# Performance work log

Hardware: AMD Instinct MI355X
Metric: run time of the kernel (lower is better)

The kernel has to match this reference:

```python
import jax, jax.numpy as jnp
import numpy as np

HID = 10  # hidden_dim


def conv1x1(x, w, b=None):
    # x: [N,C,H,W], w: [O,C] -> [N,O,H,W]
    y = jnp.einsum('oc,nchw->nohw', w, x)
    if b is not None:
        y = y + b[None, :, None, None]
    return y


def gconv1x1(x, w, b=None):
    # grouped 1x1 conv. x: [N,G*ipg,H,W], w: [G,opg,ipg]
    N, C, H, W = x.shape
    G, opg, ipg = w.shape
    xg = x.reshape(N, G, ipg, H, W)
    y = jnp.einsum('goi,ngihw->ngohw', w, xg).reshape(N, G * opg, H, W)
    if b is not None:
        y = y + b[None, :, None, None]
    return y


def _decomp(h_fea, xf, xh, att_w, att_b, w):
    # Decomposition: spatial attention from (fea, xf, xh), gate xf, project.
    att = jax.nn.sigmoid(conv1x1(jnp.concatenate([h_fea, xf, xh], axis=1), att_w, att_b))
    xfh = jax.nn.relu(conv1x1(xf * att, w))
    return xfh, att


def _comp(parts, xh, att_w, att_b, w):
    # Composition: parts [P,N,HID,H,W]; grouped per-part attention then fuse with xh.
    ca = jax.nn.sigmoid(jnp.einsum('pc,pnchw->pnhw', att_w[:, 0], parts) + att_b[:, None, None, None])
    msg = (parts * ca[:, :, None]).sum(0)  # [N,HID,H,W]
    return jax.nn.relu(conv1x1(jnp.concatenate([xh, msg], axis=1), w))


def _update(xh, m0, m1, m2, gate_w, gate_b, cand_w):
    # conv_Update: gated residual update from summed messages.
    cat = jnp.concatenate([xh, m0 + m1 + m2], axis=1)
    g = jax.nn.sigmoid(conv1x1(cat, gate_w, gate_b))
    cand = jax.nn.relu(conv1x1(cat, cand_w))
    return xh * (1.0 - g) + cand * g


def half_graph(h_fea, xh_u, xh_l, xf, xp, pdp_w1, pdp_w2, att_w, att_b,
               compU_att_w, compU_att_b, compU_w,
               compL_att_w, compL_att_b, compL_w,
               decU_att_w, decU_att_b, decU_w,
               decL_att_w, decL_att_b, decL_w,
               updU_gate_w, updU_gate_b, updU_cand_w,
               updL_gate_w, updL_gate_b, updL_cand_w):
    # Part_Dependency: shared trunk then grouped conv -> (dp_u, dp_l)
    t = jax.nn.relu(conv1x1(jnp.concatenate([h_fea, xh_u, xh_l], axis=1), pdp_w1))
    dp = jax.nn.relu(gconv1x1(t, pdp_w2))
    dp_u, dp_l = dp[:, :HID], dp[:, HID:]
    # grouped sigmoid attention over the two half nodes
    a = jax.nn.sigmoid(gconv1x1(jnp.concatenate([xh_u, xh_l], axis=1), att_w, att_b))
    ag_u, ag_l = a[:, 0:1], a[:, 1:2]
    # upper half node
    xphu = _comp(xp[0:4], xh_u, compU_att_w, compU_att_b, compU_w)
    xlh = dp_l * ag_l + xh_u * ag_u  # Pair_Part_Dependency (lower -> upper)
    xfhu, att_u = _decomp(h_fea, xf, xh_u, decU_att_w, decU_att_b, decU_w)
    xh_u_new = _update(xh_u, xphu, xlh, xfhu, updU_gate_w, updU_gate_b, updU_cand_w)
    # lower half node
    xphl = _comp(xp[4:6], xh_l, compL_att_w, compL_att_b, compL_w)
    xuh = dp_u * ag_u + xh_l * ag_l  # Pair_Part_Dependency (upper -> lower)
    xfhl, att_l = _decomp(h_fea, xf, xh_l, decL_att_w, decL_att_b, decL_w)
    xh_l_new = _update(xh_l, xphl, xuh, xfhl, updL_gate_w, updL_gate_b, updL_cand_w)
    return xh_u_new, xh_l_new, att_u, att_l


def setup_inputs() -> dict:
    key = jax.random.key(0)
    N, C, H, W = 8, 256, 128, 128
    ks = jax.random.split(key, 32)
    s = 0.05
    inp = {
        'h_fea': jax.random.normal(ks[0], (N, C, H, W), jnp.float32),
        'xh_u': jax.random.normal(ks[1], (N, HID, H, W), jnp.float32),
        'xh_l': jax.random.normal(ks[2], (N, HID, H, W), jnp.float32),
        'xf': jax.random.normal(ks[3], (N, HID, H, W), jnp.float32),
        'xp': jax.random.normal(ks[4], (6, N, HID, H, W), jnp.float32),
        'pdp_w1': jax.random.normal(ks[5], (2 * HID, C + 2 * HID), jnp.float32) * s,
        'pdp_w2': jax.random.normal(ks[6], (2, HID, HID), jnp.float32) * s,
        'att_w': jax.random.normal(ks[7], (2, 1, HID), jnp.float32) * s,
        'att_b': jnp.zeros((2,), jnp.float32),
        'compU_att_w': jax.random.normal(ks[8], (4, 1, HID), jnp.float32) * s,
        'compU_att_b': jnp.zeros((4,), jnp.float32),
        'compU_w': jax.random.normal(ks[9], (HID, 2 * HID), jnp.float32) * s,
        'compL_att_w': jax.random.normal(ks[10], (2, 1, HID), jnp.float32) * s,
        'compL_att_b': jnp.zeros((2,), jnp.float32),
        'compL_w': jax.random.normal(ks[11], (HID, 2 * HID), jnp.float32) * s,
        'decU_att_w': jax.random.normal(ks[12], (1, C + 2 * HID), jnp.float32) * s,
        'decU_att_b': jnp.zeros((1,), jnp.float32),
        'decU_w': jax.random.normal(ks[13], (HID, HID), jnp.float32) * s,
        'decL_att_w': jax.random.normal(ks[14], (1, C + 2 * HID), jnp.float32) * s,
        'decL_att_b': jnp.zeros((1,), jnp.float32),
        'decL_w': jax.random.normal(ks[15], (HID, HID), jnp.float32) * s,
        'updU_gate_w': jax.random.normal(ks[16], (HID, 2 * HID), jnp.float32) * s,
        'updU_gate_b': jnp.zeros((HID,), jnp.float32),
        'updU_cand_w': jax.random.normal(ks[17], (HID, 2 * HID), jnp.float32) * s,
        'updL_gate_w': jax.random.normal(ks[18], (HID, 2 * HID), jnp.float32) * s,
        'updL_gate_b': jnp.zeros((HID,), jnp.float32),
        'updL_cand_w': jax.random.normal(ks[19], (HID, 2 * HID), jnp.float32) * s,
    }
    return inp


def reference(h_fea, xh_u, xh_l, xf, xp, pdp_w1, pdp_w2, att_w, att_b,
              compU_att_w, compU_att_b, compU_w,
              compL_att_w, compL_att_b, compL_w,
              decU_att_w, decU_att_b, decU_w,
              decL_att_w, decL_att_b, decL_w,
              updU_gate_w, updU_gate_b, updU_cand_w,
              updL_gate_w, updL_gate_b, updL_cand_w):
    return half_graph(h_fea, xh_u, xh_l, xf, xp, pdp_w1, pdp_w2, att_w, att_b,
                      compU_att_w, compU_att_b, compU_w,
                      compL_att_w, compL_att_b, compL_w,
                      decU_att_w, decU_att_b, decU_w,
                      decL_att_w, decL_att_b, decL_w,
                      updU_gate_w, updU_gate_b, updU_cand_w,
                      updL_gate_w, updL_gate_b, updL_cand_w)
```

## Files before the change

### kernel.cpp

```cpp
#include <hip/hip_runtime.h>
#include <stdint.h>

#define HW   16384
#define NPIX 131072

typedef __attribute__((ext_vector_type(8)))  _Float16 half8;
typedef __attribute__((ext_vector_type(16))) float    f32x16;

__device__ __forceinline__ float sigm(float x) { return 1.f / (1.f + __expf(-x)); }


__global__ __launch_bounds__(256) void prep_apack(
    const float* __restrict__ pdp_w1, const float* __restrict__ dU_aw,
    const float* __restrict__ dL_aw, _Float16* __restrict__ apack)
{
    int idx = blockIdx.x * 256 + threadIdx.x;
    int s = idx >> 9, rem = idx & 511, l = rem >> 3, j = rem & 7;
    int o = l & 31, kh = l >> 5;
    int k = s * 16 + kh * 8 + j;
    float wv = 0.f;
    if (o < 20)       wv = pdp_w1[o * 276 + k];
    else if (o == 20) wv = dU_aw[k];
    else if (o == 21) wv = dL_aw[k];
    _Float16 h = (_Float16)wv;
    apack[idx]        = h;
    apack[8192 + idx] = (_Float16)(wv - (float)h);
}

__global__ __launch_bounds__(1024, 4) void half_graph_fused(
    const float* __restrict__ hf,  const float* __restrict__ xhu, const float* __restrict__ xhl,
    const float* __restrict__ xfg, const float* __restrict__ xpg,
    const float* __restrict__ pdp_w1, const float* __restrict__ pdp_w2,
    const float* __restrict__ att_w,  const float* __restrict__ att_b,
    const float* __restrict__ cU_aw, const float* __restrict__ cU_ab, const float* __restrict__ cU_w,
    const float* __restrict__ cL_aw, const float* __restrict__ cL_ab, const float* __restrict__ cL_w,
    const float* __restrict__ dU_aw, const float* __restrict__ dU_ab, const float* __restrict__ dU_w,
    const float* __restrict__ dL_aw, const float* __restrict__ dL_ab, const float* __restrict__ dL_w,
    const float* __restrict__ uU_gw, const float* __restrict__ uU_gb, const float* __restrict__ uU_cw,
    const float* __restrict__ uL_gw, const float* __restrict__ uL_gb, const float* __restrict__ uL_cw,
    const _Float16* __restrict__ apack,
    float* __restrict__ out)
{
    const int tid    = threadIdx.x;
    const int pxbase = blockIdx.x * 512;
    const int n      = pxbase >> 14;
    const int hwbase = pxbase & 16383;

    __shared__ float sacc[22][512];

    {
        const int l   = tid & 63;
        const int w   = tid >> 6;
        const int col = l & 31;
        const int kh  = l >> 5;
        const float* bp = hf + ((size_t)n * 256 + kh * 8) * HW
                             + hwbase + w * 32 + col;
        const half8* ahp = (const half8*)apack + l;
        const half8* alp = ahp + 1024;
        f32x16 acc = {};
        #pragma unroll 2
        for (int s = 0; s < 16; ++s) {
            half8 A_h = ahp[s * 64];
            half8 A_l = alp[s * 64];
            float x[8];
            #pragma unroll
            for (int j = 0; j < 8; ++j) x[j] = bp[(size_t)(s * 16 + j) * HW];
            half8 B_h, B_l;
            #pragma unroll
            for (int j = 0; j < 8; ++j) {
                _Float16 h = (_Float16)x[j];
                B_h[j] = h;
                B_l[j] = (_Float16)(x[j] - (float)h);
            }
            acc = __builtin_amdgcn_mfma_f32_32x32x16_f16(A_h, B_h, acc, 0, 0, 0);
            acc = __builtin_amdgcn_mfma_f32_32x32x16_f16(A_h, B_l, acc, 0, 0, 0);
            acc = __builtin_amdgcn_mfma_f32_32x32x16_f16(A_l, B_h, acc, 0, 0, 0);
        }
        const int ccol = w * 32 + col;
        #pragma unroll
        for (int reg = 0; reg < 12; ++reg) {
            const int r = (reg & 3) + 8 * (reg >> 2) + 4 * kh;
            if (r < 22) sacc[r][ccol] = acc[reg];
        }
    }

    const int q    = tid & 511;
    const int role = tid >> 9;
    const int hw   = hwbase + q;
    const int vb   = n * 10 * HW + hw;
    float xu[10], xl[10], xv[10];
    #pragma unroll
    for (int i = 0; i < 10; ++i) xu[i] = xhu[vb + i * HW];
    #pragma unroll
    for (int i = 0; i < 10; ++i) xl[i] = xhl[vb + i * HW];
    #pragma unroll
    for (int i = 0; i < 10; ++i) xv[i] = xfg[vb + i * HW];

    __syncthreads();

    float au_s = att_b[0], al_s = att_b[1];
    #pragma unroll
    for (int i = 0; i < 10; ++i) {
        au_s = fmaf(att_w[i],      xu[i], au_s);
        al_s = fmaf(att_w[10 + i], xl[i], al_s);
    }
    const float au = sigm(au_s), al = sigm(al_s);

    if (role == 0) {
        float tt[10];
        #pragma unroll
        for (int o = 0; o < 10; ++o) {
            const float* wr = pdp_w1 + (10 + o) * 276;
            float s = sacc[10 + o][q];
            #pragma unroll
            for (int i = 0; i < 10; ++i) s = fmaf(wr[256 + i], xu[i], s);
            #pragma unroll
            for (int i = 0; i < 10; ++i) s = fmaf(wr[266 + i], xl[i], s);
            tt[o] = fmaxf(s, 0.f);
        }
        float dpl[10];
        #pragma unroll
        for (int o = 0; o < 10; ++o) {
            float s = 0.f;
            #pragma unroll
            for (int i = 0; i < 10; ++i) s = fmaf(pdp_w2[(10 + o) * 10 + i], tt[i], s);
            dpl[o] = fmaxf(s, 0.f);
        }
        float su = sacc[20][q] + dU_ab[0];
        #pragma unroll
        for (int i = 0; i < 10; ++i) su = fmaf(dU_aw[256 + i], xv[i], su);
        #pragma unroll
        for (int i = 0; i < 10; ++i) su = fmaf(dU_aw[266 + i], xu[i], su);
        const float attU = sigm(su);
        float xfh[10];
        #pragma unroll
        for (int o = 0; o < 10; ++o) {
            float a = 0.f;
            #pragma unroll
            for (int i = 0; i < 10; ++i) a = fmaf(dU_w[o * 10 + i], xv[i], a);
            xfh[o] = fmaxf(attU * a, 0.f);
        }
        float msg[10];
        #pragma unroll
        for (int i = 0; i < 10; ++i) msg[i] = 0.f;
        #pragma unroll
        for (int pp = 0; pp < 4; ++pp) {
            const float* xq = xpg + (size_t)(pp * 8 + n) * 10 * HW + hw;
            float v[10];
            #pragma unroll
            for (int i = 0; i < 10; ++i) v[i] = xq[i * HW];
            float s = cU_ab[pp];
            #pragma unroll
            for (int i = 0; i < 10; ++i) s = fmaf(cU_aw[pp * 10 + i], v[i], s);
            float ca = sigm(s);
            #pragma unroll
            for (int i = 0; i < 10; ++i) msg[i] = fmaf(ca, v[i], msg[i]);
        }
        float m[10];
        #pragma unroll
        for (int o = 0; o < 10; ++o) {
            float s = 0.f;
            #pragma unroll
            for (int i = 0; i < 10; ++i) s = fmaf(cU_w[o * 20 + i],      xu[i],  s);
            #pragma unroll
            for (int i = 0; i < 10; ++i) s = fmaf(cU_w[o * 20 + 10 + i], msg[i], s);
            m[o] = fmaxf(s, 0.f) + fmaf(dpl[o], al, xu[o] * au) + xfh[o];
        }
        #pragma unroll
        for (int o = 0; o < 10; ++o) {
            float gs = uU_gb[o], cs = 0.f;
            #pragma unroll
            for (int i = 0; i < 10; ++i) {
                gs = fmaf(uU_gw[o * 20 + i], xu[i], gs);
                cs = fmaf(uU_cw[o * 20 + i], xu[i], cs);
            }
            #pragma unroll
            for (int i = 0; i < 10; ++i) {
                gs = fmaf(uU_gw[o * 20 + 10 + i], m[i], gs);
                cs = fmaf(uU_cw[o * 20 + 10 + i], m[i], cs);
            }
            float g = sigm(gs), cd = fmaxf(cs, 0.f);
            out[vb + o * HW] = xu[o] * (1.f - g) + cd * g;
        }
        out[2621440 + n * HW + hw] = attU;
    } else {
        float tt[10];
        #pragma unroll
        for (int o = 0; o < 10; ++o) {
            const float* wr = pdp_w1 + o * 276;
            float s = sacc[o][q];
            #pragma unroll
            for (int i = 0; i < 10; ++i) s = fmaf(wr[256 + i], xu[i], s);
            #pragma unroll
            for (int i = 0; i < 10; ++i) s = fmaf(wr[266 + i], xl[i], s);
            tt[o] = fmaxf(s, 0.f);
        }
        float dpu[10];
        #pragma unroll
        for (int o = 0; o < 10; ++o) {
            float s = 0.f;
            #pragma unroll
            for (int i = 0; i < 10; ++i) s = fmaf(pdp_w2[o * 10 + i], tt[i], s);
            dpu[o] = fmaxf(s, 0.f);
        }
        float sl = sacc[21][q] + dL_ab[0];
        #pragma unroll
        for (int i = 0; i < 10; ++i) sl = fmaf(dL_aw[256 + i], xv[i], sl);
        #pragma unroll
        for (int i = 0; i < 10; ++i) sl = fmaf(dL_aw[266 + i], xl[i], sl);
        const float attL = sigm(sl);
        float xfh[10];
        #pragma unroll
        for (int o = 0; o < 10; ++o) {
            float a = 0.f;
            #pragma unroll
            for (int i = 0; i < 10; ++i) a = fmaf(dL_w[o * 10 + i], xv[i], a);
            xfh[o] = fmaxf(attL * a, 0.f);
        }
        float msg[10];
        #pragma unroll
        for (int i = 0; i < 10; ++i) msg[i] = 0.f;
        #pragma unroll
        for (int pp = 0; pp < 2; ++pp) {
            const float* xq = xpg + (size_t)((pp + 4) * 8 + n) * 10 * HW + hw;
            float v[10];
            #pragma unroll
            for (int i = 0; i < 10; ++i) v[i] = xq[i * HW];
            float s = cL_ab[pp];
            #pragma unroll
            for (int i = 0; i < 10; ++i) s = fmaf(cL_aw[pp * 10 + i], v[i], s);
            float ca = sigm(s);
            #pragma unroll
            for (int i = 0; i < 10; ++i) msg[i] = fmaf(ca, v[i], msg[i]);
        }
        float m[10];
        #pragma unroll
        for (int o = 0; o < 10; ++o) {
            float s = 0.f;
            #pragma unroll
            for (int i = 0; i < 10; ++i) s = fmaf(cL_w[o * 20 + i],      xl[i],  s);
            #pragma unroll
            for (int i = 0; i < 10; ++i) s = fmaf(cL_w[o * 20 + 10 + i], msg[i], s);
            m[o] = fmaxf(s, 0.f) + fmaf(dpu[o], au, xl[o] * al) + xfh[o];
        }
        #pragma unroll
        for (int o = 0; o < 10; ++o) {
            float gs = uL_gb[o], cs = 0.f;
            #pragma unroll
            for (int i = 0; i < 10; ++i) {
                gs = fmaf(uL_gw[o * 20 + i], xl[i], gs);
                cs = fmaf(uL_cw[o * 20 + i], xl[i], cs);
            }
            #pragma unroll
            for (int i = 0; i < 10; ++i) {
                gs = fmaf(uL_gw[o * 20 + 10 + i], m[i], gs);
                cs = fmaf(uL_cw[o * 20 + 10 + i], m[i], cs);
            }
            float g = sigm(gs), cd = fmaxf(cs, 0.f);
            out[1310720 + vb + o * HW] = xl[o] * (1.f - g) + cd * g;
        }
        out[2752512 + n * HW + hw] = attL;
    }
}

extern "C" void kernel_launch(void* const* d_in, const int* in_sizes, int n_in,
                              void* d_out, int out_size, void* d_ws, size_t ws_size,
                              hipStream_t stream) {
    (void)in_sizes; (void)n_in; (void)out_size; (void)ws_size;
    const float* hf   = (const float*)d_in[0];
    const float* xhu  = (const float*)d_in[1];
    const float* xhl  = (const float*)d_in[2];
    const float* xfg  = (const float*)d_in[3];
    const float* xpg  = (const float*)d_in[4];
    const float* w1   = (const float*)d_in[5];
    const float* w2   = (const float*)d_in[6];
    const float* aw   = (const float*)d_in[7];
    const float* ab   = (const float*)d_in[8];
    const float* cUaw = (const float*)d_in[9];
    const float* cUab = (const float*)d_in[10];
    const float* cUw  = (const float*)d_in[11];
    const float* cLaw = (const float*)d_in[12];
    const float* cLab = (const float*)d_in[13];
    const float* cLw  = (const float*)d_in[14];
    const float* dUaw = (const float*)d_in[15];
    const float* dUab = (const float*)d_in[16];
    const float* dUw  = (const float*)d_in[17];
    const float* dLaw = (const float*)d_in[18];
    const float* dLab = (const float*)d_in[19];
    const float* dLw  = (const float*)d_in[20];
    const float* uUgw = (const float*)d_in[21];
    const float* uUgb = (const float*)d_in[22];
    const float* uUcw = (const float*)d_in[23];
    const float* uLgw = (const float*)d_in[24];
    const float* uLgb = (const float*)d_in[25];
    const float* uLcw = (const float*)d_in[26];

    _Float16* apack = (_Float16*)d_ws;

    hipLaunchKernelGGL(prep_apack, dim3(32), dim3(256), 0, stream,
                       w1, dUaw, dLaw, apack);
    hipLaunchKernelGGL(half_graph_fused, dim3(256), dim3(1024), 0, stream,
        hf, xhu, xhl, xfg, xpg, w1, w2, aw, ab,
        cUaw, cUab, cUw, cLaw, cLab, cLw,
        dUaw, dUab, dUw, dLaw, dLab, dLw,
        uUgw, uUgb, uUcw, uLgw, uLgb, uLcw,
        (const _Float16*)apack,
        (float*)d_out);
}
```

Baseline: 285.6 us.

## Stage h_fea through LDS with vectorized prefetch and halve block pixel tile

Replaces the per-lane strided scalar global loads of h_fea with float4 coalesced loads into an LDS staging buffer, double-buffered via register prefetch of the next 32-channel chunk while MFMAs consume the current one. Blocks now cover 256 pixels with 512 threads and the grid doubles to 512 blocks, which raises the number of blocks in flight. It adds two barriers per chunk and extra LDS traffic. The tail of the kernel is reindexed for the smaller tile.

```diff
diff --git a/kernel.cpp b/kernel.cpp
--- a/kernel.cpp
+++ b/kernel.cpp
@@ -4,6 +4,7 @@
 #define HW   16384
 #define NPIX 131072
 
+typedef __attribute__((ext_vector_type(4)))  float    f32x4;
 typedef __attribute__((ext_vector_type(8)))  _Float16 half8;
 typedef __attribute__((ext_vector_type(16))) float    f32x16;
 
@@ -27,7 +28,7 @@
     apack[8192 + idx] = (_Float16)(wv - (float)h);
 }
 
-__global__ __launch_bounds__(1024, 4) void half_graph_fused(
+__global__ __launch_bounds__(512, 4) void half_graph_fused(
     const float* __restrict__ hf,  const float* __restrict__ xhu, const float* __restrict__ xhl,
     const float* __restrict__ xfg, const float* __restrict__ xpg,
     const float* __restrict__ pdp_w1, const float* __restrict__ pdp_w2,
@@ -42,39 +43,68 @@
     float* __restrict__ out)
 {
     const int tid    = threadIdx.x;
-    const int pxbase = blockIdx.x * 512;
+    const int pxbase = blockIdx.x * 256;
     const int n      = pxbase >> 14;
     const int hwbase = pxbase & 16383;
 
-    __shared__ float sacc[22][512];
+    __shared__ float lstage[32][256];
+    __shared__ float sacc[22][256];
 
     {
         const int l   = tid & 63;
         const int w   = tid >> 6;
         const int col = l & 31;
         const int kh  = l >> 5;
-        const float* bp = hf + ((size_t)n * 256 + kh * 8) * HW
-                             + hwbase + w * 32 + col;
         const half8* ahp = (const half8*)apack + l;
         const half8* alp = ahp + 1024;
+        const float* hfb = hf + (size_t)n * 256 * HW + hwbase;
+
         f32x16 acc = {};
-        #pragma unroll 2
-        for (int s = 0; s < 16; ++s) {
-            half8 A_h = ahp[s * 64];
-            half8 A_l = alp[s * 64];
-            float x[8];
-            #pragma unroll
-            for (int j = 0; j < 8; ++j) x[j] = bp[(size_t)(s * 16 + j) * HW];
-            half8 B_h, B_l;
-            #pragma unroll
-            for (int j = 0; j < 8; ++j) {
-                _Float16 h = (_Float16)x[j];
-                B_h[j] = h;
-                B_l[j] = (_Float16)(x[j] - (float)h);
-            }
-            acc = __builtin_amdgcn_mfma_f32_32x32x16_f16(A_h, B_h, acc, 0, 0, 0);
-            acc = __builtin_amdgcn_mfma_f32_32x32x16_f16(A_h, B_l, acc, 0, 0, 0);
-            acc = __builtin_amdgcn_mfma_f32_32x32x16_f16(A_l, B_h, acc, 0, 0, 0);
+        f32x4 pf[4];
+        #pragma unroll
+        for (int i = 0; i < 4; ++i) {
+            int fid = i * 512 + tid;
+            int ch = fid >> 6, f = fid & 63;
+            pf[i] = *(const f32x4*)&hfb[(size_t)ch * HW + f * 4];
+        }
+        for (int c = 0; c < 8; ++c) {
+            #pragma unroll
+            for (int i = 0; i < 4; ++i) {
+                int fid = i * 512 + tid;
+                int ch = fid >> 6, f = fid & 63;
+                *(f32x4*)&lstage[ch][f * 4] = pf[i];
+            }
+            __syncthreads();
+            if (c < 7) {
+                const float* src = hfb + (size_t)(c + 1) * 32 * HW;
+                #pragma unroll
+                for (int i = 0; i < 4; ++i) {
+                    int fid = i * 512 + tid;
+                    int ch = fid >> 6, f = fid & 63;
+                    pf[i] = *(const f32x4*)&src[(size_t)ch * HW + f * 4];
+                }
+            }
+            #pragma unroll
+            for (int s = 0; s < 2; ++s) {
+                const int S = c * 2 + s;
+                half8 A_h = ahp[S * 64];
+                half8 A_l = alp[S * 64];
+                float x[8];
+                #pragma unroll
+                for (int j = 0; j < 8; ++j)
+                    x[j] = lstage[s * 16 + kh * 8 + j][w * 32 + col];
+                half8 B_h, B_l;
+                #pragma unroll
+                for (int j = 0; j < 8; ++j) {
+                    _Float16 h = (_Float16)x[j];
+                    B_h[j] = h;
+                    B_l[j] = (_Float16)(x[j] - (float)h);
+                }
+                acc = __builtin_amdgcn_mfma_f32_32x32x16_f16(A_h, B_h, acc, 0, 0, 0);
+                acc = __builtin_amdgcn_mfma_f32_32x32x16_f16(A_h, B_l, acc, 0, 0, 0);
+                acc = __builtin_amdgcn_mfma_f32_32x32x16_f16(A_l, B_h, acc, 0, 0, 0);
+            }
+            __syncthreads();
         }
         const int ccol = w * 32 + col;
         #pragma unroll
@@ -84,8 +114,8 @@
         }
     }
 
-    const int q    = tid & 511;
-    const int role = tid >> 9;
+    const int q    = tid & 255;
+    const int role = tid >> 8;
     const int hw   = hwbase + q;
     const int vb   = n * 10 * HW + hw;
     float xu[10], xl[10], xv[10];
@@ -299,7 +329,7 @@
 
     hipLaunchKernelGGL(prep_apack, dim3(32), dim3(256), 0, stream,
                        w1, dUaw, dLaw, apack);
-    hipLaunchKernelGGL(half_graph_fused, dim3(256), dim3(1024), 0, stream,
+    hipLaunchKernelGGL(half_graph_fused, dim3(512), dim3(512), 0, stream,
         hf, xhu, xhl, xfg, xpg, w1, w2, aw, ab,
         cUaw, cUab, cUw, cLaw, cLab, cLw,
         dUaw, dUab, dUw, dLaw, dLab, dLw,
```

Measured after the change: 276.1 us. 1.03x faster.

## Double-buffer hf channel chunks into LDS via async global_load_lds, halve block tile

Applied to the files above, without the earlier changes.

The MFMA trunk no longer reads hf straight from global memory with strided per-lane loads. It stages 16-channel chunks into a double-buffered LDS tile using the direct global-to-LDS load builtin, prefetching the next chunk while the current one is computed. Blocks shrink to 512 threads covering 256 pixels, and the grid doubles to 512. The goal is wider coalesced loads and overlap of memory latency with compute. The cost is a __syncthreads per chunk and extra LDS, and it relies on the compiler inserting the right wait before LDS reads of the async loads.

```diff
diff --git a/kernel.cpp b/kernel.cpp
--- a/kernel.cpp
+++ b/kernel.cpp
@@ -8,6 +8,13 @@
 typedef __attribute__((ext_vector_type(16))) float    f32x16;
 
 __device__ __forceinline__ float sigm(float x) { return 1.f / (1.f + __expf(-x)); }
+
+__device__ __forceinline__ void gl_lds16(const float* g, float* l) {
+    __builtin_amdgcn_global_load_lds(
+        (const __attribute__((address_space(1))) unsigned int*)g,
+        (__attribute__((address_space(3)))       unsigned int*)l,
+        16, 0, 0);
+}
 
 
 __global__ __launch_bounds__(256) void prep_apack(
@@ -27,7 +34,7 @@
     apack[8192 + idx] = (_Float16)(wv - (float)h);
 }
 
-__global__ __launch_bounds__(1024, 4) void half_graph_fused(
+__global__ __launch_bounds__(512, 4) void half_graph_fused(
     const float* __restrict__ hf,  const float* __restrict__ xhu, const float* __restrict__ xhl,
     const float* __restrict__ xfg, const float* __restrict__ xpg,
     const float* __restrict__ pdp_w1, const float* __restrict__ pdp_w2,
@@ -42,29 +49,43 @@
     float* __restrict__ out)
 {
     const int tid    = threadIdx.x;
-    const int pxbase = blockIdx.x * 512;
+    const int pxbase = blockIdx.x * 256;
     const int n      = pxbase >> 14;
     const int hwbase = pxbase & 16383;
 
-    __shared__ float sacc[22][512];
+    __shared__ float lstage[2][16][256];
+    __shared__ float sacc[22][256];
 
     {
         const int l   = tid & 63;
         const int w   = tid >> 6;
         const int col = l & 31;
         const int kh  = l >> 5;
-        const float* bp = hf + ((size_t)n * 256 + kh * 8) * HW
-                             + hwbase + w * 32 + col;
         const half8* ahp = (const half8*)apack + l;
         const half8* alp = ahp + 1024;
+        const float* hfb = hf + (size_t)n * 256 * HW + hwbase;
+
+        auto stage = [&](int c, int buf) {
+            #pragma unroll
+            for (int i = 0; i < 2; ++i) {
+                const int chl = i * 8 + w;
+                gl_lds16(hfb + (size_t)(c * 16 + chl) * HW + l * 4,
+                         &lstage[buf][chl][0]);
+            }
+        };
+
         f32x16 acc = {};
-        #pragma unroll 2
-        for (int s = 0; s < 16; ++s) {
-            half8 A_h = ahp[s * 64];
-            half8 A_l = alp[s * 64];
+        stage(0, 0);
+        for (int c = 0; c < 16; ++c) {
+            __syncthreads();
+            if (c < 15) stage(c + 1, (c + 1) & 1);
+            const int b = c & 1;
+            half8 A_h = ahp[c * 64];
+            half8 A_l = alp[c * 64];
             float x[8];
             #pragma unroll
-            for (int j = 0; j < 8; ++j) x[j] = bp[(size_t)(s * 16 + j) * HW];
+            for (int j = 0; j < 8; ++j)
+                x[j] = lstage[b][kh * 8 + j][w * 32 + col];
             half8 B_h, B_l;
             #pragma unroll
             for (int j = 0; j < 8; ++j) {
@@ -84,8 +105,8 @@
         }
     }
 
-    const int q    = tid & 511;
-    const int role = tid >> 9;
+    const int q    = tid & 255;
+    const int role = tid >> 8;
     const int hw   = hwbase + q;
     const int vb   = n * 10 * HW + hw;
     float xu[10], xl[10], xv[10];
@@ -299,7 +320,7 @@
 
     hipLaunchKernelGGL(prep_apack, dim3(32), dim3(256), 0, stream,
                        w1, dUaw, dLaw, apack);
-    hipLaunchKernelGGL(half_graph_fused, dim3(256), dim3(1024), 0, stream,
+    hipLaunchKernelGGL(half_graph_fused, dim3(512), dim3(512), 0, stream,
         hf, xhu, xhl, xfg, xpg, w1, w2, aw, ab,
         cUaw, cUab, cUw, cLaw, cLab, cLw,
         dUaw, dUab, dUw, dLaw, dLab, dLw,
```

Result: faster. 277.5 us (-2.9%).
